# Performance work log

Hardware: AMD Instinct MI355X
Metric: run time of the kernel (lower is better)

## Reference

```python
import jax, jax.numpy as jnp
import numpy as np

EPS = 1e-12  # torch F.normalize default eps


def setup_inputs() -> dict:
    key = jax.random.key(0)
    ks = jax.random.split(key, 5)
    b, c, h, w = 2, 192, 256, 256
    x = jax.random.normal(ks[0], (b, c, h, w), dtype=jnp.float32)
    temperature = jnp.ones((1, 1, 1), dtype=jnp.float32)
    qkv_w = jax.random.normal(ks[1], (3 * c, c), dtype=jnp.float32) * 0.02
    qkv_b = jax.random.normal(ks[2], (3 * c,), dtype=jnp.float32) * 0.02
    proj_w = jax.random.normal(ks[3], (c, c), dtype=jnp.float32) * 0.02
    proj_b = jax.random.normal(ks[4], (c,), dtype=jnp.float32) * 0.02
    return {"x": x, "temperature": temperature, "qkv_w": qkv_w, "qkv_b": qkv_b,
            "proj_w": proj_w, "proj_b": proj_b}


def reference(x, temperature, qkv_w, qkv_b, proj_w, proj_b):
    b, c, h, w = x.shape
    n = h * w
    # [b, c, h, w] -> [b, n, c] tokens over spatial, features = channels
    xt = x.reshape(b, c, n).transpose(0, 2, 1)
    qkv = xt @ qkv_w.T + qkv_b                     # [b, n, 3c]
    q, k, v = jnp.split(qkv, 3, axis=-1)           # each [b, n, c]
    q = q.transpose(0, 2, 1)                       # [b, c, n]
    k = k.transpose(0, 2, 1)
    v = v.transpose(0, 2, 1)
    # L2 normalize along spatial (last) dim, torch-style clamp
    q = q / jnp.maximum(jnp.linalg.norm(q, axis=-1, keepdims=True), EPS)
    k = k / jnp.maximum(jnp.linalg.norm(k, axis=-1, keepdims=True), EPS)
    attn = jnp.einsum('bcn,bdn->bcd', q, k) * temperature[0, 0, 0]  # [b, c, c]
    attn = jax.nn.softmax(attn, axis=-1)
    out = jnp.einsum('bcd,bdn->bcn', attn, v)      # [b, c, n]
    out = out.reshape(b, c, h, w)
    # 1x1 conv projection = channel matmul
    out = jnp.einsum('bchw,dc->bdhw', out, proj_w) + proj_b[None, :, None, None]
    return out
```

## Files before the change

### kernel.cpp

```cpp
#include <hip/hip_runtime.h>
#include <hip/hip_bf16.h>
#include <stdint.h>

typedef __attribute__((ext_vector_type(8))) __bf16 bf16x8;
typedef __attribute__((ext_vector_type(4))) float f32x4;
typedef __attribute__((ext_vector_type(4))) uint u32x4;

#define C192 192
#define NSP 65536
#define EPS_N 1e-12f

#define SLICE_ELEMS 20224
#define ONES_OFF_E 19968

__device__ __forceinline__ uint32_t f2bf1(float a){
  uint32_t u = __float_as_uint(a);
  return (u + 0x7fffu + ((u >> 16) & 1u)) >> 16;
}
__device__ __forceinline__ uint32_t f2bf2(float lo, float hi){
  return f2bf1(lo) | (f2bf1(hi) << 16);
}
__device__ __forceinline__ float bf2f(ushort u){
  return __uint_as_float(((uint32_t)u) << 16);
}

__global__ __launch_bounds__(768, 4) void k_gram(const float* __restrict__ x,
                                                 ushort* __restrict__ gpart){
  __shared__ float xs[2 * 6144];
  char* lb = (char*)xs;
  const int tid = threadIdx.x;
  const int lane = tid & 63, wid = tid >> 6;
  const int l15 = lane & 15, hi = lane >> 4;
  const int b = blockIdx.x >> 7, slice = blockIdx.x & 127;
  const int j0 = slice * 512;

  const int p = (wid < 6) ? wid : (wid - 6);
  const int nFirst = 5 - p;
  const float* xg = x + ((size_t)b * C192) * NSP + j0;

  const int swcol = ((lane & 7) ^ (lane >> 3)) * 4;
  const float* srow = xg + (size_t)(wid * 16 + (lane >> 3)) * NSP + swcol;

  auto ISSUE = [&](int c, int bi){
    char* dst = lb + bi * 24576 + wid * 2048;
    const float* s0 = srow + c * 32;
    const float* s1 = s0 + (size_t)8 * NSP;
    __builtin_amdgcn_global_load_lds((__attribute__((address_space(1))) const void*)s0,
                                     (__attribute__((address_space(3))) void*)(dst), 16, 0, 0);
    __builtin_amdgcn_global_load_lds((__attribute__((address_space(1))) const void*)s1,
                                     (__attribute__((address_space(3))) void*)(dst + 1024), 16, 0, 0);
  };

  f32x4 acc[8];
  #pragma unroll
  for (int t = 0; t < 8; t++) acc[t] = (f32x4){0.f, 0.f, 0.f, 0.f};

  uint ov = (l15 == 0) ? 0x3F803F80u : 0u;
  u32x4 oq = {ov, ov, ov, ov};
  bf16x8 onesf = __builtin_bit_cast(bf16x8, oq);

  auto LOADFRAG = [&](const char* base, int row) -> bf16x8 {
    int sw = (row & 7) << 4;
    f32x4 v0 = *(const f32x4*)(base + row * 128 + ((hi * 32) ^ sw));
    f32x4 v1 = *(const f32x4*)(base + row * 128 + ((hi * 32 + 16) ^ sw));
    uint w0, w1, w2, w3;
    asm("v_cvt_pk_bf16_f32 %0, %1, %2" : "=v"(w0) : "v"(v0.x), "v"(v0.y));
    asm("v_cvt_pk_bf16_f32 %0, %1, %2" : "=v"(w1) : "v"(v0.z), "v"(v0.w));
    asm("v_cvt_pk_bf16_f32 %0, %1, %2" : "=v"(w2) : "v"(v1.x), "v"(v1.y));
    asm("v_cvt_pk_bf16_f32 %0, %1, %2" : "=v"(w3) : "v"(v1.z), "v"(v1.w));
    u32x4 q = {w0, w1, w2, w3};
    return __builtin_bit_cast(bf16x8, q);
  };

  auto COMPUTE = [&](int bi){
    const char* base = lb + bi * 24576;
    bf16x8 a0 = LOADFRAG(base, p * 16 + l15);
    bf16x8 a1 = (wid >= 6) ? LOADFRAG(base, (11 - p) * 16 + l15) : a0;
    #pragma unroll
    for (int t = 0; t < 8; t++){
      if (wid >= 6 && t >= 7) break;
      int j = (wid < 6) ? (p + t) : ((t < nFirst) ? (p + 8 + t) : (t + 6));
      bf16x8 bf = (j < 12) ? LOADFRAG(base, j * 16 + l15) : onesf;
      bf16x8 aS = (wid < 6 || t < nFirst) ? a0 : a1;
      acc[t] = __builtin_amdgcn_mfma_f32_16x16x32_bf16(aS, bf, acc[t], 0, 0, 0);
    }
  };

  ISSUE(0, 0);
  for (int c = 0; c < 16; c++){
    __syncthreads();
    if (c < 15) ISSUE(c + 1, (c + 1) & 1);
    COMPUTE(c & 1);
  }

  ushort* gp = gpart + (size_t)(b * 128 + slice) * SLICE_ELEMS;
  #pragma unroll
  for (int t = 0; t < 8; t++){
    if (wid >= 6 && t >= 7) break;
    int i = (wid < 6) ? p : ((t < nFirst) ? p : (11 - p));
    int j = (wid < 6) ? (p + t) : ((t < nFirst) ? (p + 8 + t) : (t + 6));
    uint2 u2;
    u2.x = f2bf2(acc[t][0], acc[t][1]);
    u2.y = f2bf2(acc[t][2], acc[t][3]);
    if (j < 12){
      int F = 12 * i - (i * (i - 1)) / 2 + (j - i);
      *(uint2*)(gp + F * 256 + lane * 4) = u2;
    } else if (l15 == 0){
      *(uint2*)(gp + ONES_OFF_E + i * 16 + hi * 4) = u2;
    }
  }
}

__global__ __launch_bounds__(1024) void k_reduce(const ushort* __restrict__ gpart,
                                                 float* __restrict__ gaug,
                                                 const float* __restrict__ qkv_w,
                                                 float* __restrict__ wkT){
  int blk = blockIdx.x, tid = threadIdx.x;
  if (blk < 180){
    __shared__ float red[4][256];
    int b = blk / 90, slot = blk % 90;
    int q = tid >> 8, e = tid & 255;
    float sum = 0.f;
    if (slot < 78){
      const ushort* pp = gpart + (size_t)(b * 128 + q) * SLICE_ELEMS + slot * 256 + e;
      #pragma unroll 8
      for (int k2 = 0; k2 < 32; k2++) sum += bf2f(pp[(size_t)k2 * (4 * SLICE_ELEMS)]);
    } else if (e < 16){
      int i = slot - 78;
      const ushort* pp = gpart + (size_t)(b * 128 + q) * SLICE_ELEMS + ONES_OFF_E + i * 16 + e;
      #pragma unroll 8
      for (int k2 = 0; k2 < 32; k2++) sum += bf2f(pp[(size_t)k2 * (4 * SLICE_ELEMS)]);
    }
    red[q][e] = sum;
    __syncthreads();
    if (tid < 256){
      float tot = red[0][tid] + red[1][tid] + red[2][tid] + red[3][tid];
      if (slot < 78){
        int i = 0, off = 0;
        while (slot >= off + (12 - i)){ off += 12 - i; i++; }
        int j = i + (slot - off);
        int e2 = tid;
        int row = ((e2 >> 6) << 2) | (e2 & 3);
        int col = (e2 >> 2) & 15;
        int R = i * 16 + row, Cc = j * 16 + col;
        gaug[((size_t)b * C192 + R) * 193 + Cc] = tot;
        gaug[((size_t)b * C192 + Cc) * 193 + R] = tot;
      } else if (tid < 16){
        int i = slot - 78;
        gaug[((size_t)b * C192 + i * 16 + tid) * 193 + 192] = tot;
      }
    }
  } else {
    int idx = (blk - 180) * 1024 + tid;
    if (idx < 36864){
      int d = idx / 192, e = idx % 192;
      wkT[e * 192 + d] = qkv_w[(192 + d) * 192 + e];
    }
  }
}

__global__ __launch_bounds__(256) void k_pr(const float* __restrict__ gaug,
                                            const float* __restrict__ qkv_w,
                                            const float* __restrict__ qkv_b,
                                            float* __restrict__ pr,
                                            float* __restrict__ norms){
  __shared__ float red[4];
  __shared__ float uSh;
  int blk = blockIdx.x, tid = threadIdx.x;
  int b = blk / 384, which = (blk / 192) % 2, c = blk % 192;
  const float* wrow = qkv_w + (which * 192 + c) * 192;
  float acc = 0.f;
  if (tid < 193){
    const float* g = gaug + (size_t)b * C192 * 193 + tid;
    #pragma unroll 4
    for (int e = 0; e < 192; e++) acc += wrow[e] * g[(size_t)e * 193];
    pr[(((size_t)b * 2 + which) * 192 + c) * 193 + tid] = acc;
  }
  if (tid == 192) uSh = acc;
  float v = (tid < 192) ? acc * wrow[tid] : 0.f;
  for (int o = 32; o > 0; o >>= 1) v += __shfl_down(v, o, 64);
  if ((tid & 63) == 0) red[tid >> 6] = v;
  __syncthreads();
  if (tid == 0){
    float s = red[0] + red[1] + red[2] + red[3];
    float bias = qkv_b[which * 192 + c];
    float n2 = s + 2.f * bias * uSh + 65536.f * bias * bias;
    norms[(b * 2 + which) * 192 + c] = fmaxf(sqrtf(fmaxf(n2, 0.f)), EPS_N);
  }
}

__global__ __launch_bounds__(256) void k_attn_u(const float* __restrict__ pr,
                                                const float* __restrict__ wkT,
                                                const float* __restrict__ norms,
                                                const float* __restrict__ qkv_b,
                                                const float* __restrict__ temperature,
                                                const float* __restrict__ qkv_w,
                                                float* __restrict__ uaug){
  __shared__ float Pc[193];
  __shared__ float red[4];
  __shared__ float bcast;
  int blk = blockIdx.x, tid = threadIdx.x;
  int b = blk / 192, c = blk % 192;
  if (tid < 193) Pc[tid] = pr[(((size_t)b * 2 + 0) * 192 + c) * 193 + tid];
  __syncthreads();
  int d = tid;
  float logit = -1e30f, pv = 0.f;
  if (d < 192){
    float sS = 0.f;
    #pragma unroll 4
    for (int e = 0; e < 192; e++) sS += Pc[e] * wkT[e * 192 + d];
    float bq = qkv_b[c], bk = qkv_b[192 + d];
    float w2 = pr[(((size_t)b * 2 + 1) * 192 + d) * 193 + 192];
    float Sv = sS + Pc[192] * bk + bq * w2 + 65536.f * bq * bk;
    float nq = norms[(b * 2 + 0) * 192 + c];
    float nk = norms[(b * 2 + 1) * 192 + d];
    logit = temperature[0] * Sv / (nq * nk);
  }
  float m = logit;
  for (int o = 32; o > 0; o >>= 1) m = fmaxf(m, __shfl_down(m, o, 64));
  if ((tid & 63) == 0) red[tid >> 6] = m;
  __syncthreads();
  if (tid == 0) bcast = fmaxf(fmaxf(red[0], red[1]), fmaxf(red[2], red[3]));
  __syncthreads();
  m = bcast;
  pv = (d < 192) ? __expf(logit - m) : 0.f;
  float s = pv;
  for (int o = 32; o > 0; o >>= 1) s += __shfl_down(s, o, 64);
  __syncthreads();
  if ((tid & 63) == 0) red[tid >> 6] = s;
  __syncthreads();
  if (tid == 0) bcast = red[0] + red[1] + red[2] + red[3];
  __syncthreads();
  float aw = (d < 192) ? (pv / bcast) : 0.f;
  __syncthreads();
  if (d < 192) Pc[d] = aw;
  __syncthreads();
  int e = tid;
  if (e <= 192){
    float acc = 0.f;
    if (e < 192){
      #pragma unroll 4
      for (int d2 = 0; d2 < 192; d2++) acc += Pc[d2] * qkv_w[(384 + d2) * 192 + e];
    } else {
      #pragma unroll 4
      for (int d2 = 0; d2 < 192; d2++) acc += Pc[d2] * qkv_b[384 + d2];
    }
    uaug[((size_t)b * 192 + c) * 193 + e] = acc;
  }
}

__global__ __launch_bounds__(256) void k_f(const float* __restrict__ uaug,
                                           const float* __restrict__ proj_w,
                                           const float* __restrict__ proj_b,
                                           ushort* __restrict__ fb,
                                           float* __restrict__ gvec){
  __shared__ float pw[192];
  int blk = blockIdx.x, tid = threadIdx.x;
  int b = blk / 192, f = blk % 192;
  if (tid < 192) pw[tid] = proj_w[f * 192 + tid];
  __syncthreads();
  int e = tid;
  if (e <= 192){
    float acc = 0.f;
    const float* u = uaug + (size_t)b * 192 * 193 + e;
    #pragma unroll 4
    for (int c2 = 0; c2 < 192; c2++) acc += pw[c2] * u[(size_t)c2 * 193];
    if (e < 192) fb[((size_t)b * 192 + f) * 192 + e] = (ushort)f2bf1(acc);
    else gvec[b * 192 + f] = acc + proj_b[f];
  }
}

__global__ __launch_bounds__(256, 3) void k_out(const float* __restrict__ x,
                                                const ushort* __restrict__ fb,
                                                const float* __restrict__ gvec,
                                                float* __restrict__ out){
  __shared__ ushort xt[128 * 192];
  char* lb = (char*)xt;
  const int tid = threadIdx.x;
  const int lane = tid & 63, wid = tid >> 6;
  const int l15 = lane & 15, hi = lane >> 4;
  const int b = blockIdx.x >> 9, cb = blockIdx.x & 511;
  const int j0 = cb * 128;

  const float* xg = x + ((size_t)b * C192) * NSP + j0;
  #pragma unroll
  for (int half = 0; half < 2; half++){
    float4 ra[12];
    #pragma unroll
    for (int ii = 0; ii < 3; ii++){
      int unit = (half * 3 + ii) * 256 + tid;
      int cp = unit >> 4, s8 = unit & 15;
      int c0 = cp * 2, sp0 = s8 * 8;
      const float* r0 = xg + (size_t)c0 * NSP + sp0;
      const float* r1 = xg + (size_t)(c0 + 1) * NSP + sp0;
      ra[4 * ii]     = *(const float4*)(r0);
      ra[4 * ii + 1] = *(const float4*)(r0 + 4);
      ra[4 * ii + 2] = *(const float4*)(r1);
      ra[4 * ii + 3] = *(const float4*)(r1 + 4);
    }
    #pragma unroll
    for (int ii = 0; ii < 3; ii++){
      int unit = (half * 3 + ii) * 256 + tid;
      int cp = unit >> 4, s8 = unit & 15;
      int c0 = cp * 2, sp0 = s8 * 8;
      float fa[8] = {ra[4*ii].x, ra[4*ii].y, ra[4*ii].z, ra[4*ii].w,
                     ra[4*ii+1].x, ra[4*ii+1].y, ra[4*ii+1].z, ra[4*ii+1].w};
      float fc[8] = {ra[4*ii+2].x, ra[4*ii+2].y, ra[4*ii+2].z, ra[4*ii+2].w,
                     ra[4*ii+3].x, ra[4*ii+3].y, ra[4*ii+3].z, ra[4*ii+3].w};
      #pragma unroll
      for (int s = 0; s < 8; s++){
        int sp = sp0 + s;
        int byte = sp * 384 + c0 * 2;
        byte ^= (((sp & 7) ^ ((sp >> 3) & 7)) << 4);
        uint pk;
        asm("v_cvt_pk_bf16_f32 %0, %1, %2" : "=v"(pk) : "v"(fa[s]), "v"(fc[s]));
        *(uint*)(lb + byte) = pk;
      }
    }
  }

  float gv[3];
  #pragma unroll
  for (int i = 0; i < 3; i++)
    gv[i] = gvec[b * 192 + (wid * 3 + i) * 16 + l15];

  f32x4 acc[3][8];
  #pragma unroll
  for (int i = 0; i < 3; i++)
    #pragma unroll
    for (int j = 0; j < 8; j++)
      acc[i][j] = (f32x4){0.f, 0.f, 0.f, 0.f};

  __syncthreads();

  for (int k = 0; k < 6; k++){
    bf16x8 bF[3];
    #pragma unroll
    for (int i = 0; i < 3; i++){
      const ushort* fr = fb + ((size_t)b * 192 + (wid * 3 + i) * 16 + l15) * 192;
      bF[i] = *(const bf16x8*)(fr + k * 32 + hi * 8);
    }
    #pragma unroll
    for (int ct = 0; ct < 8; ct++){
      int sp = ct * 16 + l15;
      int byte = sp * 384 + k * 64 + hi * 16;
      byte ^= (((sp & 7) ^ ((sp >> 3) & 7)) << 4);
      bf16x8 aX = *(const bf16x8*)(lb + byte);
      #pragma unroll
      for (int i = 0; i < 3; i++)
        acc[i][ct] = __builtin_amdgcn_mfma_f32_16x16x32_bf16(aX, bF[i], acc[i][ct], 0, 0, 0);
    }
  }

  #pragma unroll
  for (int i = 0; i < 3; i++){
    int chan = (wid * 3 + i) * 16 + l15;
    float* ob = out + ((size_t)b * C192 + chan) * NSP + j0;
    #pragma unroll
    for (int ct = 0; ct < 8; ct++){
      float4 v;
      v.x = acc[i][ct][0] + gv[i];
      v.y = acc[i][ct][1] + gv[i];
      v.z = acc[i][ct][2] + gv[i];
      v.w = acc[i][ct][3] + gv[i];
      *(float4*)(ob + ct * 16 + hi * 4) = v;
    }
  }
}

extern "C" void kernel_launch(void* const* d_in, const int* in_sizes, int n_in,
                              void* d_out, int out_size, void* d_ws, size_t ws_size,
                              hipStream_t stream){
  const float* x           = (const float*)d_in[0];
  const float* temperature = (const float*)d_in[1];
  const float* qkv_w       = (const float*)d_in[2];
  const float* qkv_b       = (const float*)d_in[3];
  const float* proj_w      = (const float*)d_in[4];
  const float* proj_b      = (const float*)d_in[5];
  float* out = (float*)d_out;
  char* ws = (char*)d_ws;

  ushort* gpart = (ushort*)(ws);
  float*  gaug  = (float*) (ws + 10354688);
  float*  pr    = (float*) (ws + 10651136);
  float*  wkT   = (float*) (ws + 11244032);
  float*  norms = (float*) (ws + 11391488);
  float*  uaug  = (float*) (ws + 11394560);
  ushort* fb    = (ushort*)(ws + 11691008);
  float*  gvec  = (float*) (ws + 11838464);

  hipLaunchKernelGGL(k_gram,   dim3(256),  dim3(768),  0, stream, x, gpart);
  hipLaunchKernelGGL(k_reduce, dim3(216),  dim3(1024), 0, stream, gpart, gaug, qkv_w, wkT);
  hipLaunchKernelGGL(k_pr,     dim3(768),  dim3(256),  0, stream, gaug, qkv_w, qkv_b, pr, norms);
  hipLaunchKernelGGL(k_attn_u, dim3(384),  dim3(256),  0, stream, pr, wkT, norms, qkv_b, temperature, qkv_w, uaug);
  hipLaunchKernelGGL(k_f,      dim3(384),  dim3(256),  0, stream, uaug, proj_w, proj_b, fb, gvec);
  hipLaunchKernelGGL(k_out,    dim3(1024), dim3(256),  0, stream, x, fb, gvec, out);
}
```

Baseline: 126.7 us.

## Fuse middle small kernels into one cooperative kernel with grid syncs

Replaces the four small kernels between the gram and output stages (reduce, pr/norms, attention-softmax, projection fold) with a single cooperative launch of 384 blocks that separates the phases with grid-wide syncs. Each block now handles two units in the pr phase, and the reduce phase runs with 256 threads, each doing a serial 128-term sum. The aim is to remove launch gaps and tail latency between the tiny dependent kernels. The costs are grid-sync overhead, a cooperative launch that needs every block resident at once, and a slower reduce phase because it has fewer threads.

```diff
diff --git a/kernel.cpp b/kernel.cpp
--- a/kernel.cpp
+++ b/kernel.cpp
@@ -1,6 +1,9 @@
 #include <hip/hip_runtime.h>
 #include <hip/hip_bf16.h>
+#include <hip/hip_cooperative_groups.h>
 #include <stdint.h>
+
+namespace cg = cooperative_groups;
 
 typedef __attribute__((ext_vector_type(8))) __bf16 bf16x8;
 typedef __attribute__((ext_vector_type(4))) float f32x4;
@@ -111,162 +114,149 @@
   }
 }
 
-__global__ __launch_bounds__(1024) void k_reduce(const ushort* __restrict__ gpart,
-                                                 float* __restrict__ gaug,
-                                                 const float* __restrict__ qkv_w,
-                                                 float* __restrict__ wkT){
-  int blk = blockIdx.x, tid = threadIdx.x;
-  if (blk < 180){
-    __shared__ float red[4][256];
-    int b = blk / 90, slot = blk % 90;
-    int q = tid >> 8, e = tid & 255;
-    float sum = 0.f;
-    if (slot < 78){
-      const ushort* pp = gpart + (size_t)(b * 128 + q) * SLICE_ELEMS + slot * 256 + e;
-      #pragma unroll 8
-      for (int k2 = 0; k2 < 32; k2++) sum += bf2f(pp[(size_t)k2 * (4 * SLICE_ELEMS)]);
-    } else if (e < 16){
-      int i = slot - 78;
-      const ushort* pp = gpart + (size_t)(b * 128 + q) * SLICE_ELEMS + ONES_OFF_E + i * 16 + e;
-      #pragma unroll 8
-      for (int k2 = 0; k2 < 32; k2++) sum += bf2f(pp[(size_t)k2 * (4 * SLICE_ELEMS)]);
-    }
-    red[q][e] = sum;
-    __syncthreads();
-    if (tid < 256){
-      float tot = red[0][tid] + red[1][tid] + red[2][tid] + red[3][tid];
-      if (slot < 78){
-        int i = 0, off = 0;
-        while (slot >= off + (12 - i)){ off += 12 - i; i++; }
-        int j = i + (slot - off);
-        int e2 = tid;
-        int row = ((e2 >> 6) << 2) | (e2 & 3);
-        int col = (e2 >> 2) & 15;
-        int R = i * 16 + row, Cc = j * 16 + col;
-        gaug[((size_t)b * C192 + R) * 193 + Cc] = tot;
-        gaug[((size_t)b * C192 + Cc) * 193 + R] = tot;
-      } else if (tid < 16){
-        int i = slot - 78;
-        gaug[((size_t)b * C192 + i * 16 + tid) * 193 + 192] = tot;
-      }
-    }
-  } else {
-    int idx = (blk - 180) * 1024 + tid;
-    if (idx < 36864){
-      int d = idx / 192, e = idx % 192;
-      wkT[e * 192 + d] = qkv_w[(192 + d) * 192 + e];
-    }
-  }
-}
-
-__global__ __launch_bounds__(256) void k_pr(const float* __restrict__ gaug,
-                                            const float* __restrict__ qkv_w,
-                                            const float* __restrict__ qkv_b,
-                                            float* __restrict__ pr,
-                                            float* __restrict__ norms){
-  __shared__ float red[4];
-  __shared__ float uSh;
-  int blk = blockIdx.x, tid = threadIdx.x;
-  int b = blk / 384, which = (blk / 192) % 2, c = blk % 192;
-  const float* wrow = qkv_w + (which * 192 + c) * 192;
-  float acc = 0.f;
-  if (tid < 193){
-    const float* g = gaug + (size_t)b * C192 * 193 + tid;
-    #pragma unroll 4
-    for (int e = 0; e < 192; e++) acc += wrow[e] * g[(size_t)e * 193];
-    pr[(((size_t)b * 2 + which) * 192 + c) * 193 + tid] = acc;
-  }
-  if (tid == 192) uSh = acc;
-  float v = (tid < 192) ? acc * wrow[tid] : 0.f;
-  for (int o = 32; o > 0; o >>= 1) v += __shfl_down(v, o, 64);
-  if ((tid & 63) == 0) red[tid >> 6] = v;
-  __syncthreads();
-  if (tid == 0){
-    float s = red[0] + red[1] + red[2] + red[3];
-    float bias = qkv_b[which * 192 + c];
-    float n2 = s + 2.f * bias * uSh + 65536.f * bias * bias;
-    norms[(b * 2 + which) * 192 + c] = fmaxf(sqrtf(fmaxf(n2, 0.f)), EPS_N);
-  }
-}
-
-__global__ __launch_bounds__(256) void k_attn_u(const float* __restrict__ pr,
-                                                const float* __restrict__ wkT,
-                                                const float* __restrict__ norms,
-                                                const float* __restrict__ qkv_b,
-                                                const float* __restrict__ temperature,
-                                                const float* __restrict__ qkv_w,
-                                                float* __restrict__ uaug){
+__global__ __launch_bounds__(256) void k_mid(const ushort* __restrict__ gpart,
+                                             float* __restrict__ gaug,
+                                             const float* __restrict__ qkv_w,
+                                             float* __restrict__ wkT,
+                                             const float* __restrict__ qkv_b,
+                                             float* __restrict__ pr,
+                                             float* __restrict__ norms,
+                                             const float* __restrict__ temperature,
+                                             float* __restrict__ uaug,
+                                             const float* __restrict__ proj_w,
+                                             const float* __restrict__ proj_b,
+                                             ushort* __restrict__ fb,
+                                             float* __restrict__ gvec){
+  cg::grid_group grid = cg::this_grid();
   __shared__ float Pc[193];
   __shared__ float red[4];
   __shared__ float bcast;
-  int blk = blockIdx.x, tid = threadIdx.x;
-  int b = blk / 192, c = blk % 192;
-  if (tid < 193) Pc[tid] = pr[(((size_t)b * 2 + 0) * 192 + c) * 193 + tid];
-  __syncthreads();
-  int d = tid;
-  float logit = -1e30f, pv = 0.f;
-  if (d < 192){
-    float sS = 0.f;
-    #pragma unroll 4
-    for (int e = 0; e < 192; e++) sS += Pc[e] * wkT[e * 192 + d];
-    float bq = qkv_b[c], bk = qkv_b[192 + d];
-    float w2 = pr[(((size_t)b * 2 + 1) * 192 + d) * 193 + 192];
-    float Sv = sS + Pc[192] * bk + bq * w2 + 65536.f * bq * bk;
-    float nq = norms[(b * 2 + 0) * 192 + c];
-    float nk = norms[(b * 2 + 1) * 192 + d];
-    logit = temperature[0] * Sv / (nq * nk);
-  }
-  float m = logit;
-  for (int o = 32; o > 0; o >>= 1) m = fmaxf(m, __shfl_down(m, o, 64));
-  if ((tid & 63) == 0) red[tid >> 6] = m;
-  __syncthreads();
-  if (tid == 0) bcast = fmaxf(fmaxf(red[0], red[1]), fmaxf(red[2], red[3]));
-  __syncthreads();
-  m = bcast;
-  pv = (d < 192) ? __expf(logit - m) : 0.f;
-  float s = pv;
-  for (int o = 32; o > 0; o >>= 1) s += __shfl_down(s, o, 64);
-  __syncthreads();
-  if ((tid & 63) == 0) red[tid >> 6] = s;
-  __syncthreads();
-  if (tid == 0) bcast = red[0] + red[1] + red[2] + red[3];
-  __syncthreads();
-  float aw = (d < 192) ? (pv / bcast) : 0.f;
-  __syncthreads();
-  if (d < 192) Pc[d] = aw;
-  __syncthreads();
-  int e = tid;
-  if (e <= 192){
+  __shared__ float uSh;
+  __shared__ float pw[192];
+  const int blk = blockIdx.x, tid = threadIdx.x;
+
+  if (blk < 180){
+    int b = blk / 90, slot = blk % 90;
+    int e = tid;
+    if (slot < 78){
+      float sum = 0.f;
+      const ushort* pp = gpart + (size_t)(b * 128) * SLICE_ELEMS + slot * 256 + e;
+      #pragma unroll 8
+      for (int k2 = 0; k2 < 128; k2++) sum += bf2f(pp[(size_t)k2 * SLICE_ELEMS]);
+      int i = 0, off = 0;
+      while (slot >= off + (12 - i)){ off += 12 - i; i++; }
+      int j = i + (slot - off);
+      int row = ((e >> 6) << 2) | (e & 3);
+      int col = (e >> 2) & 15;
+      int R = i * 16 + row, Cc = j * 16 + col;
+      gaug[((size_t)b * C192 + R) * 193 + Cc] = sum;
+      gaug[((size_t)b * C192 + Cc) * 193 + R] = sum;
+    } else if (e < 16){
+      int i = slot - 78;
+      float sum = 0.f;
+      const ushort* pp = gpart + (size_t)(b * 128) * SLICE_ELEMS + ONES_OFF_E + i * 16 + e;
+      #pragma unroll 8
+      for (int k2 = 0; k2 < 128; k2++) sum += bf2f(pp[(size_t)k2 * SLICE_ELEMS]);
+      gaug[((size_t)b * C192 + i * 16 + e) * 193 + 192] = sum;
+    }
+  } else if (blk < 324){
+    int idx = (blk - 180) * 256 + tid;
+    int d = idx / 192, e2 = idx % 192;
+    wkT[e2 * 192 + d] = qkv_w[(192 + d) * 192 + e2];
+  }
+  grid.sync();
+
+  #pragma unroll
+  for (int rep = 0; rep < 2; rep++){
+    int unit = blk * 2 + rep;
+    int b = unit / 384, which = (unit / 192) % 2, c = unit % 192;
+    const float* wrow = qkv_w + (which * 192 + c) * 192;
     float acc = 0.f;
-    if (e < 192){
+    if (tid < 193){
+      const float* g = gaug + (size_t)b * C192 * 193 + tid;
       #pragma unroll 4
-      for (int d2 = 0; d2 < 192; d2++) acc += Pc[d2] * qkv_w[(384 + d2) * 192 + e];
-    } else {
+      for (int e = 0; e < 192; e++) acc += wrow[e] * g[(size_t)e * 193];
+      pr[(((size_t)b * 2 + which) * 192 + c) * 193 + tid] = acc;
+    }
+    if (tid == 192) uSh = acc;
+    float v = (tid < 192) ? acc * wrow[tid] : 0.f;
+    for (int o = 32; o > 0; o >>= 1) v += __shfl_down(v, o, 64);
+    if ((tid & 63) == 0) red[tid >> 6] = v;
+    __syncthreads();
+    if (tid == 0){
+      float s = red[0] + red[1] + red[2] + red[3];
+      float bias = qkv_b[which * 192 + c];
+      float n2 = s + 2.f * bias * uSh + 65536.f * bias * bias;
+      norms[(b * 2 + which) * 192 + c] = fmaxf(sqrtf(fmaxf(n2, 0.f)), EPS_N);
+    }
+    __syncthreads();
+  }
+  grid.sync();
+
+  {
+    int b = blk / 192, c = blk % 192;
+    if (tid < 193) Pc[tid] = pr[(((size_t)b * 2 + 0) * 192 + c) * 193 + tid];
+    __syncthreads();
+    int d = tid;
+    float logit = -1e30f, pv = 0.f;
+    if (d < 192){
+      float sS = 0.f;
       #pragma unroll 4
-      for (int d2 = 0; d2 < 192; d2++) acc += Pc[d2] * qkv_b[384 + d2];
-    }
-    uaug[((size_t)b * 192 + c) * 193 + e] = acc;
-  }
-}
-
-__global__ __launch_bounds__(256) void k_f(const float* __restrict__ uaug,
-                                           const float* __restrict__ proj_w,
-                                           const float* __restrict__ proj_b,
-                                           ushort* __restrict__ fb,
-                                           float* __restrict__ gvec){
-  __shared__ float pw[192];
-  int blk = blockIdx.x, tid = threadIdx.x;
-  int b = blk / 192, f = blk % 192;
-  if (tid < 192) pw[tid] = proj_w[f * 192 + tid];
-  __syncthreads();
-  int e = tid;
-  if (e <= 192){
-    float acc = 0.f;
-    const float* u = uaug + (size_t)b * 192 * 193 + e;
-    #pragma unroll 4
-    for (int c2 = 0; c2 < 192; c2++) acc += pw[c2] * u[(size_t)c2 * 193];
-    if (e < 192) fb[((size_t)b * 192 + f) * 192 + e] = (ushort)f2bf1(acc);
-    else gvec[b * 192 + f] = acc + proj_b[f];
+      for (int e = 0; e < 192; e++) sS += Pc[e] * wkT[e * 192 + d];
+      float bq = qkv_b[c], bk = qkv_b[192 + d];
+      float w2 = pr[(((size_t)b * 2 + 1) * 192 + d) * 193 + 192];
+      float Sv = sS + Pc[192] * bk + bq * w2 + 65536.f * bq * bk;
+      float nq = norms[(b * 2 + 0) * 192 + c];
+      float nk = norms[(b * 2 + 1) * 192 + d];
+      logit = temperature[0] * Sv / (nq * nk);
+    }
+    float m = logit;
+    for (int o = 32; o > 0; o >>= 1) m = fmaxf(m, __shfl_down(m, o, 64));
+    if ((tid & 63) == 0) red[tid >> 6] = m;
+    __syncthreads();
+    if (tid == 0) bcast = fmaxf(fmaxf(red[0], red[1]), fmaxf(red[2], red[3]));
+    __syncthreads();
+    m = bcast;
+    pv = (d < 192) ? __expf(logit - m) : 0.f;
+    float s = pv;
+    for (int o = 32; o > 0; o >>= 1) s += __shfl_down(s, o, 64);
+    __syncthreads();
+    if ((tid & 63) == 0) red[tid >> 6] = s;
+    __syncthreads();
+    if (tid == 0) bcast = red[0] + red[1] + red[2] + red[3];
+    __syncthreads();
+    float aw = (d < 192) ? (pv / bcast) : 0.f;
+    __syncthreads();
+    if (d < 192) Pc[d] = aw;
+    __syncthreads();
+    int e = tid;
+    if (e <= 192){
+      float acc = 0.f;
+      if (e < 192){
+        #pragma unroll 4
+        for (int d2 = 0; d2 < 192; d2++) acc += Pc[d2] * qkv_w[(384 + d2) * 192 + e];
+      } else {
+        #pragma unroll 4
+        for (int d2 = 0; d2 < 192; d2++) acc += Pc[d2] * qkv_b[384 + d2];
+      }
+      uaug[((size_t)b * 192 + c) * 193 + e] = acc;
+    }
+  }
+  grid.sync();
+
+  {
+    int b = blk / 192, f = blk % 192;
+    if (tid < 192) pw[tid] = proj_w[f * 192 + tid];
+    __syncthreads();
+    int e = tid;
+    if (e <= 192){
+      float acc = 0.f;
+      const float* u = uaug + (size_t)b * 192 * 193 + e;
+      #pragma unroll 4
+      for (int c2 = 0; c2 < 192; c2++) acc += pw[c2] * u[(size_t)c2 * 193];
+      if (e < 192) fb[((size_t)b * 192 + f) * 192 + e] = (ushort)f2bf1(acc);
+      else gvec[b * 192 + f] = acc + proj_b[f];
+    }
   }
 }
 
@@ -389,10 +379,13 @@
   ushort* fb    = (ushort*)(ws + 11691008);
   float*  gvec  = (float*) (ws + 11838464);
 
-  hipLaunchKernelGGL(k_gram,   dim3(256),  dim3(768),  0, stream, x, gpart);
-  hipLaunchKernelGGL(k_reduce, dim3(216),  dim3(1024), 0, stream, gpart, gaug, qkv_w, wkT);
-  hipLaunchKernelGGL(k_pr,     dim3(768),  dim3(256),  0, stream, gaug, qkv_w, qkv_b, pr, norms);
-  hipLaunchKernelGGL(k_attn_u, dim3(384),  dim3(256),  0, stream, pr, wkT, norms, qkv_b, temperature, qkv_w, uaug);
-  hipLaunchKernelGGL(k_f,      dim3(384),  dim3(256),  0, stream, uaug, proj_w, proj_b, fb, gvec);
-  hipLaunchKernelGGL(k_out,    dim3(1024), dim3(256),  0, stream, x, fb, gvec, out);
-}
+  hipLaunchKernelGGL(k_gram, dim3(256), dim3(768), 0, stream, x, gpart);
+
+  void* args[] = {(void*)&gpart, (void*)&gaug, (void*)&qkv_w, (void*)&wkT,
+                  (void*)&qkv_b, (void*)&pr, (void*)&norms, (void*)&temperature,
+                  (void*)&uaug, (void*)&proj_w, (void*)&proj_b, (void*)&fb,
+                  (void*)&gvec};
+  hipLaunchCooperativeKernel((void*)k_mid, dim3(384), dim3(256), args, 0, stream);
+
+  hipLaunchKernelGGL(k_out, dim3(1024), dim3(256), 0, stream, x, fb, gvec, out);
+}
```

New measurement: 271.3 us. 2.14x slower.
